# Performance work log

Hardware: AMD Instinct MI355X
Metric: run time of the kernel (lower is better)

## Reference

```python
import jax, jax.numpy as jnp
import numpy as np


def setup_inputs() -> dict:
    key = jax.random.key(0)
    k_x, k_q, k_k, k_v = jax.random.split(key, 4)
    B, S, D = 8, 1024, 768
    H, DH = 12, 64
    scale = 1.0 / np.sqrt(D)
    return {
        "x": jax.random.normal(k_x, (B, S, D), dtype=jnp.float32),
        "Wq": jax.random.normal(k_q, (H, D, DH), dtype=jnp.float32) * scale,
        "Wk": jax.random.normal(k_k, (H, D, DH), dtype=jnp.float32) * scale,
        "Wv": jax.random.normal(k_v, (H, D, DH), dtype=jnp.float32) * scale,
    }


def reference(x, Wq, Wk, Wv):
    # x: [B, S, D]; Wq/Wk/Wv: [H, D, DH] (per-head Linear weights, no bias)
    B, S, D = x.shape
    H, _, DH = Wq.shape
    q = jnp.einsum("bsd,hde->bhse", x, Wq)  # [B,H,S,DH]
    k = jnp.einsum("bsd,hde->bhse", x, Wk)
    v = jnp.einsum("bsd,hde->bhse", x, Wv)
    scores = jnp.einsum("bhse,bhte->bhst", q, k) / jnp.sqrt(jnp.float32(DH))
    causal = jnp.tril(jnp.ones((S, S), dtype=bool))  # keep lower triangle
    scores = jnp.where(causal, scores, -jnp.inf)
    attn = jax.nn.softmax(scores, axis=-1)  # dropout = 0.0 -> identity
    ctx = jnp.einsum("bhst,bhte->bhse", attn, v)  # [B,H,S,DH]
    # concat heads on last dim: [B,S,H*DH]
    return ctx.transpose(0, 2, 1, 3).reshape(B, S, H * DH)
```

## Files before the change

kernel.cpp:

```cpp
#include <hip/hip_runtime.h>


#define Bq 8
#define Sq 1024
#define Dq 768
#define Hq 12
#define DHq 64

typedef _Float16 f16;
typedef f16 f16x8 __attribute__((ext_vector_type(8)));
typedef float f32x4 __attribute__((ext_vector_type(4)));

#define MFMA16(a, b, c) __builtin_amdgcn_mfma_f32_16x16x32_f16(a, b, c, 0, 0, 0)

#define QSCL 0.1803368801111244f

#if __has_builtin(__builtin_amdgcn_exp2f)
#define EXP2(x) __builtin_amdgcn_exp2f(x)
#else
#define EXP2(x) exp2f(x)
#endif

__device__ __forceinline__ void gload16(const f16* g, f16* l) {
  __builtin_amdgcn_global_load_lds(
      (const __attribute__((address_space(1))) void*)g,
      (__attribute__((address_space(3))) void*)l, 16, 0, 0);
}

__global__ __launch_bounds__(256) void cvt_x_kernel(const float* __restrict__ x,
                                                    f16* __restrict__ xh) {
  int i = blockIdx.x * 256 + threadIdx.x;
  const float4* src = reinterpret_cast<const float4*>(x) + i * 2;
  float4 a = src[0], b = src[1];
  f16x8 o;
  o[0] = (f16)a.x; o[1] = (f16)a.y; o[2] = (f16)a.z; o[3] = (f16)a.w;
  o[4] = (f16)b.x; o[5] = (f16)b.y; o[6] = (f16)b.z; o[7] = (f16)b.w;
  *reinterpret_cast<f16x8*>(xh + i * 8) = o;
}

__global__ __launch_bounds__(256) void cvt_w_kernel(const float* __restrict__ Wq,
                                                    const float* __restrict__ Wk,
                                                    const float* __restrict__ Wv,
                                                    f16* __restrict__ WT) {
  __shared__ float tile[64][65];
  const int kt = blockIdx.x, h = blockIdx.y, w = blockIdx.z;
  const float* W = (w == 0) ? Wq : (w == 1) ? Wk : Wv;
  const int t = threadIdx.x;
  const int c0 = t & 63, r4 = t >> 6;
#pragma unroll
  for (int i = 0; i < 16; i++) {
    int kr = i * 4 + r4;
    tile[kr][c0] = W[((size_t)h * Dq + kt * 64 + kr) * DHq + c0];
  }
  __syncthreads();
#pragma unroll
  for (int i = 0; i < 16; i++) {
    int e2 = i * 4 + r4;
    WT[((size_t)(w * Hq + h) * DHq + e2) * Dq + kt * 64 + c0] = (f16)tile[c0][e2];
  }
}

__global__ __launch_bounds__(256) void proj_kernel(const f16* __restrict__ xh,
                                                   const f16* __restrict__ WT,
                                                   f16* __restrict__ Q,
                                                   f16* __restrict__ K,
                                                   f16* __restrict__ Vt) {
  __shared__ __align__(1024) f16 smem[30720];

  const int mt = blockIdx.x;
  const int h = blockIdx.y;
  const int row0 = mt * 128;
  const int t = threadIdx.x;
  const int wv = t >> 6;
  const int lane = t & 63;
  const int g = lane >> 4;
  const int ql = lane & 15;
  const int wvm = wv >> 1, wvn = wv & 1;

  const int lr = lane >> 2;
  const int scg = (lane & 3) ^ ((lane >> 3) & 3);

  const f16* xsrc = xh + (size_t)row0 * Dq;
  const f16* wsrc = WT + (size_t)h * DHq * Dq;

  const f16* gA0 = xsrc + (size_t)(wv * 32 + lr) * Dq + scg * 8;
  const f16* gA1 = gA0 + (size_t)16 * Dq;
  const int n0 = wv * 48 + lr, n1 = n0 + 16, n2 = n0 + 32;
  const f16* gB0 = wsrc + ((size_t)(n0 >> 6) * Hq * DHq + (n0 & 63)) * Dq + scg * 8;
  const f16* gB1 = wsrc + ((size_t)(n1 >> 6) * Hq * DHq + (n1 & 63)) * Dq + scg * 8;
  const f16* gB2 = wsrc + ((size_t)(n2 >> 6) * Hq * DHq + (n2 & 63)) * Dq + scg * 8;

  f32x4 acc[4][6] = {};

#define PROJ_STAGE(buf)                                              \
  do {                                                               \
    f16* sA_ = smem + (buf) * 4096 + wv * 1024;                      \
    f16* sB_ = smem + 12288 + (buf) * 6144 + wv * 1536;              \
    gload16(gA0, sA_); gload16(gA1, sA_ + 512);                      \
    gload16(gB0, sB_); gload16(gB1, sB_ + 512);                      \
    gload16(gB2, sB_ + 1024);                                        \
    gA0 += 32; gA1 += 32; gB0 += 32; gB1 += 32; gB2 += 32;           \
  } while (0)

  PROJ_STAGE(0);
  PROJ_STAGE(1);

  const int rq = (g ^ ((ql >> 1) & 3)) * 8;
  const f16* rA = smem + (wvm * 64 + ql) * 32 + rq;
  const f16* rB = smem + 12288 + (wvn * 96 + ql) * 32 + rq;

#pragma unroll
  for (int step = 0; step < 24; step++) {
    if (step < 23) asm volatile("s_waitcnt vmcnt(5) lgkmcnt(0)" ::: "memory");
    else           asm volatile("s_waitcnt vmcnt(0) lgkmcnt(0)" ::: "memory");
    __builtin_amdgcn_s_barrier();
    __builtin_amdgcn_sched_barrier(0);
    if (step < 22) PROJ_STAGE((step + 2) % 3);
    const int cur = step % 3;
    f16x8 af[4], bf[6];
#pragma unroll
    for (int mf = 0; mf < 4; mf++)
      af[mf] = *reinterpret_cast<const f16x8*>(rA + cur * 4096 + mf * 512);
#pragma unroll
    for (int nf = 0; nf < 6; nf++)
      bf[nf] = *reinterpret_cast<const f16x8*>(rB + cur * 6144 + nf * 512);
    __builtin_amdgcn_s_setprio(1);
#pragma unroll
    for (int mf = 0; mf < 4; mf++)
#pragma unroll
      for (int nf = 0; nf < 6; nf++)
        acc[mf][nf] = MFMA16(af[mf], bf[nf], acc[mf][nf]);
    __builtin_amdgcn_s_setprio(0);
  }
#undef PROJ_STAGE
  __syncthreads();

  const int b = row0 >> 10;
  const int s0 = row0 & 1023;
  const size_t base_sd = ((size_t)(b * Hq + h) * Sq) * DHq;

#pragma unroll
  for (int nf = 0; nf < 6; nf++) {
    const int c = wvn * 96 + nf * 16 + ql;
    const int w = c >> 6;
    if (w < 2) {
      f16* dst = (w == 0 ? Q : K);
      const float scl = (w == 0) ? QSCL : 1.0f;
      const int e = c & 63;
#pragma unroll
      for (int mf = 0; mf < 4; mf++) {
        const int sr = wvm * 64 + mf * 16 + g * 4;
#pragma unroll
        for (int r = 0; r < 4; r++)
          dst[base_sd + (size_t)(s0 + sr + r) * DHq + e] = (f16)(acc[mf][nf][r] * scl);
      }
    }
  }

  f16* vbuf = smem;
#pragma unroll
  for (int nf = 2; nf < 6; nf++) {
    if (wvn == 1) {
      const int e = (96 + nf * 16 + ql) & 63;
#pragma unroll
      for (int mf = 0; mf < 4; mf++) {
        const int sr = wvm * 64 + mf * 16 + g * 4;
        union { f16 hh[4]; uint2 u; } z;
#pragma unroll
        for (int r = 0; r < 4; r++) z.hh[r] = (f16)acc[mf][nf][r];
        *reinterpret_cast<uint2*>(&vbuf[e * 136 + sr]) = z.u;
      }
    }
  }
  __syncthreads();
#pragma unroll
  for (int i = 0; i < 4; i++) {
    int c = t + 256 * i;
    int e = c >> 4, p = (c & 15) * 8;
    *reinterpret_cast<uint4*>(Vt + base_sd + (size_t)e * Sq + s0 + p) =
        *reinterpret_cast<const uint4*>(vbuf + e * 136 + p);
  }
}

__global__ __launch_bounds__(256) void attn_kernel(const f16* __restrict__ Q,
                                                   const f16* __restrict__ K,
                                                   const f16* __restrict__ Vt,
                                                   float* __restrict__ out) {
  __shared__ __align__(16) f16 k_lds[2][64][72];
  __shared__ __align__(16) f16 vt_lds[2][64][72];

  const int L = blockIdx.x;
  const int i = L >> 3;
  const int bh = (L & 7) * Hq + (i % Hq);
  const int mt = 15 - (i / Hq);
  const int t = threadIdx.x;
  const int wv = t >> 6;
  const int lane = t & 63;
  const int g = lane >> 4;
  const int ql = lane & 15;

  const f16* Qb = Q + (size_t)bh * Sq * DHq;
  const f16* Kb = K + (size_t)bh * Sq * DHq;
  const f16* Vtb = Vt + (size_t)bh * DHq * Sq;
  const int b = bh / Hq, h = bh % Hq;

  const int r0 = t >> 3;
  const int p0 = (t & 7) * 8;

  const int q0 = mt * 64;
  const int qg = q0 + wv * 16 + ql;
  f16x8 qf0 = *reinterpret_cast<const f16x8*>(Qb + (size_t)qg * DHq + g * 8);
  f16x8 qf1 = *reinterpret_cast<const f16x8*>(Qb + (size_t)qg * DHq + 32 + g * 8);

  f32x4 o_acc[4] = {};
  float m_r = -__builtin_inff(), l_r = 0.f;

  uint4 kreg0, kreg1, vreg0, vreg1;
  kreg0 = *reinterpret_cast<const uint4*>(Kb + (size_t)r0 * DHq + p0);
  kreg1 = *reinterpret_cast<const uint4*>(Kb + (size_t)(32 + r0) * DHq + p0);
  vreg0 = *reinterpret_cast<const uint4*>(Vtb + (size_t)r0 * Sq + p0);
  vreg1 = *reinterpret_cast<const uint4*>(Vtb + (size_t)(32 + r0) * Sq + p0);
  *reinterpret_cast<uint4*>(&k_lds[0][r0][p0]) = kreg0;
  *reinterpret_cast<uint4*>(&k_lds[0][32 + r0][p0]) = kreg1;
  *reinterpret_cast<uint4*>(&vt_lds[0][r0][p0]) = vreg0;
  *reinterpret_cast<uint4*>(&vt_lds[0][32 + r0][p0]) = vreg1;
  if (mt >= 1) {
    kreg0 = *reinterpret_cast<const uint4*>(Kb + (size_t)(64 + r0) * DHq + p0);
    kreg1 = *reinterpret_cast<const uint4*>(Kb + (size_t)(96 + r0) * DHq + p0);
    vreg0 = *reinterpret_cast<const uint4*>(Vtb + (size_t)r0 * Sq + 64 + p0);
    vreg1 = *reinterpret_cast<const uint4*>(Vtb + (size_t)(32 + r0) * Sq + 64 + p0);
  }
  __syncthreads();

  int cur = 0;
  for (int kt = 0; kt <= mt; kt++) {
    f32x4 sf[4] = {};
    __builtin_amdgcn_s_setprio(1);
#pragma unroll
    for (int nt = 0; nt < 4; nt++) {
      f16x8 kf0 = *reinterpret_cast<const f16x8*>(&k_lds[cur][nt * 16 + ql][g * 8]);
      f16x8 kf1 = *reinterpret_cast<const f16x8*>(&k_lds[cur][nt * 16 + ql][32 + g * 8]);
      sf[nt] = MFMA16(kf0, qf0, sf[nt]);
      sf[nt] = MFMA16(kf1, qf1, sf[nt]);
    }
    __builtin_amdgcn_s_setprio(0);

    if (kt == mt) {
#pragma unroll
      for (int nt = 0; nt < 4; nt++)
#pragma unroll
        for (int r = 0; r < 4; r++)
          if (nt * 16 + g * 4 + r > wv * 16 + ql) sf[nt][r] = -__builtin_inff();
    }

    float t0 = fmaxf(fmaxf(sf[0][0], sf[0][1]), fmaxf(sf[0][2], sf[0][3]));
    float t1 = fmaxf(fmaxf(sf[1][0], sf[1][1]), fmaxf(sf[1][2], sf[1][3]));
    float t2 = fmaxf(fmaxf(sf[2][0], sf[2][1]), fmaxf(sf[2][2], sf[2][3]));
    float t3 = fmaxf(fmaxf(sf[3][0], sf[3][1]), fmaxf(sf[3][2], sf[3][3]));
    float rowmax = fmaxf(fmaxf(t0, t1), fmaxf(t2, t3));
    rowmax = fmaxf(rowmax, __shfl_xor(rowmax, 16, 64));
    rowmax = fmaxf(rowmax, __shfl_xor(rowmax, 32, 64));

    if (!__all(rowmax <= m_r + 8.f)) {
      float mnew = fmaxf(m_r, rowmax);
      float corr = EXP2(m_r - mnew);
      l_r *= corr;
#pragma unroll
      for (int nt = 0; nt < 4; nt++) {
        o_acc[nt][0] *= corr; o_acc[nt][1] *= corr;
        o_acc[nt][2] *= corr; o_acc[nt][3] *= corr;
      }
      m_r = mnew;
    }

    float p[4][4];
#pragma unroll
    for (int nt = 0; nt < 4; nt++)
#pragma unroll
      for (int r = 0; r < 4; r++) p[nt][r] = EXP2(sf[nt][r] - m_r);
    float s0 = (p[0][0] + p[0][1]) + (p[0][2] + p[0][3]);
    float s1 = (p[1][0] + p[1][1]) + (p[1][2] + p[1][3]);
    float s2 = (p[2][0] + p[2][1]) + (p[2][2] + p[2][3]);
    float s3 = (p[3][0] + p[3][1]) + (p[3][2] + p[3][3]);
    float rs = (s0 + s1) + (s2 + s3);
    rs += __shfl_xor(rs, 16, 64);
    rs += __shfl_xor(rs, 32, 64);
    l_r += rs;

    uint32_t pk[4][2];
#pragma unroll
    for (int nt = 0; nt < 4; nt++) {
      union { f16 hh[2]; uint32_t u; } z0, z1;
      z0.hh[0] = (f16)p[nt][0]; z0.hh[1] = (f16)p[nt][1];
      z1.hh[0] = (f16)p[nt][2]; z1.hh[1] = (f16)p[nt][3];
      pk[nt][0] = z0.u; pk[nt][1] = z1.u;
    }
    const int srcA = ((g & 1) * 2) * 16 + ql;
    const int srcB = srcA + 16;
    const bool selhi = (g >> 1) != 0;
    f16x8 pf[2];
#pragma unroll
    for (int ks = 0; ks < 2; ks++) {
      uint32_t aA0 = (uint32_t)__shfl((int)pk[2 * ks][0], srcA, 64);
      uint32_t aA1 = (uint32_t)__shfl((int)pk[2 * ks][1], srcA, 64);
      uint32_t aB0 = (uint32_t)__shfl((int)pk[2 * ks][0], srcB, 64);
      uint32_t aB1 = (uint32_t)__shfl((int)pk[2 * ks][1], srcB, 64);
      uint32_t bA0 = (uint32_t)__shfl((int)pk[2 * ks + 1][0], srcA, 64);
      uint32_t bA1 = (uint32_t)__shfl((int)pk[2 * ks + 1][1], srcA, 64);
      uint32_t bB0 = (uint32_t)__shfl((int)pk[2 * ks + 1][0], srcB, 64);
      uint32_t bB1 = (uint32_t)__shfl((int)pk[2 * ks + 1][1], srcB, 64);
      union { uint32_t w[4]; f16x8 v; } z;
      z.w[0] = selhi ? bA0 : aA0;
      z.w[1] = selhi ? bA1 : aA1;
      z.w[2] = selhi ? bB0 : aB0;
      z.w[3] = selhi ? bB1 : aB1;
      pf[ks] = z.v;
    }

    __builtin_amdgcn_s_setprio(1);
#pragma unroll
    for (int nt = 0; nt < 4; nt++) {
      f16x8 vf0 = *reinterpret_cast<const f16x8*>(&vt_lds[cur][nt * 16 + ql][g * 8]);
      f16x8 vf1 = *reinterpret_cast<const f16x8*>(&vt_lds[cur][nt * 16 + ql][32 + g * 8]);
      o_acc[nt] = MFMA16(vf0, pf[0], o_acc[nt]);
      o_acc[nt] = MFMA16(vf1, pf[1], o_acc[nt]);
    }
    __builtin_amdgcn_s_setprio(0);

    if (kt < mt) {
      *reinterpret_cast<uint4*>(&k_lds[cur ^ 1][r0][p0]) = kreg0;
      *reinterpret_cast<uint4*>(&k_lds[cur ^ 1][32 + r0][p0]) = kreg1;
      *reinterpret_cast<uint4*>(&vt_lds[cur ^ 1][r0][p0]) = vreg0;
      *reinterpret_cast<uint4*>(&vt_lds[cur ^ 1][32 + r0][p0]) = vreg1;
      if (kt + 2 <= mt) {
        const int kv0 = (kt + 2) * 64;
        kreg0 = *reinterpret_cast<const uint4*>(Kb + (size_t)(kv0 + r0) * DHq + p0);
        kreg1 = *reinterpret_cast<const uint4*>(Kb + (size_t)(kv0 + 32 + r0) * DHq + p0);
        vreg0 = *reinterpret_cast<const uint4*>(Vtb + (size_t)r0 * Sq + kv0 + p0);
        vreg1 = *reinterpret_cast<const uint4*>(Vtb + (size_t)(32 + r0) * Sq + kv0 + p0);
      }
    }
    __syncthreads();
    cur ^= 1;
  }

  float rl = 1.0f / l_r;
  float* op = out + ((size_t)(b * Sq + qg)) * (Hq * DHq) + h * DHq;
#pragma unroll
  for (int nt = 0; nt < 4; nt++) {
    float4 st = { o_acc[nt][0] * rl, o_acc[nt][1] * rl,
                  o_acc[nt][2] * rl, o_acc[nt][3] * rl };
    *reinterpret_cast<float4*>(op + nt * 16 + g * 4) = st;
  }
}

extern "C" void kernel_launch(void* const* d_in, const int* in_sizes, int n_in,
                              void* d_out, int out_size, void* d_ws, size_t ws_size,
                              hipStream_t stream) {
  const float* x = (const float*)d_in[0];
  const float* Wq = (const float*)d_in[1];
  const float* Wk = (const float*)d_in[2];
  const float* Wv = (const float*)d_in[3];
  float* out = (float*)d_out;

  const size_t off_xb = 0;
  const size_t off_wt = 12582912;
  const size_t off_q = 16121856;
  const size_t off_k = 28704768;
  const size_t off_v = 41287680;
  const size_t need = 53870592;
  if (ws_size < need) return;

  char* ws = (char*)d_ws;
  f16* xh = (f16*)(ws + off_xb);
  f16* WT = (f16*)(ws + off_wt);
  f16* Qd = (f16*)(ws + off_q);
  f16* Kd = (f16*)(ws + off_k);
  f16* Vtd = (f16*)(ws + off_v);

  cvt_x_kernel<<<3072, 256, 0, stream>>>(x, xh);
  cvt_w_kernel<<<dim3(12, 12, 3), 256, 0, stream>>>(Wq, Wk, Wv, WT);
  proj_kernel<<<dim3(64, 12), 256, 0, stream>>>(xh, WT, Qd, Kd, Vtd);
  attn_kernel<<<1536, 256, 0, stream>>>(Qd, Kd, Vtd, out);
}
```

Baseline: 86.35 us.

## Load K/V MFMA fragments directly from global memory, dropping LDS staging

```diff
diff --git a/kernel.cpp b/kernel.cpp
--- a/kernel.cpp
+++ b/kernel.cpp
@@ -186,9 +186,6 @@
                                                    const f16* __restrict__ K,
                                                    const f16* __restrict__ Vt,
                                                    float* __restrict__ out) {
-  __shared__ __align__(16) f16 k_lds[2][64][72];
-  __shared__ __align__(16) f16 vt_lds[2][64][72];
-
   const int L = blockIdx.x;
   const int i = L >> 3;
   const int bh = (L & 7) * Hq + (i % Hq);
@@ -204,44 +201,38 @@
   const f16* Vtb = Vt + (size_t)bh * DHq * Sq;
   const int b = bh / Hq, h = bh % Hq;
 
-  const int r0 = t >> 3;
-  const int p0 = (t & 7) * 8;
-
-  const int q0 = mt * 64;
-  const int qg = q0 + wv * 16 + ql;
+  const int qg = mt * 64 + wv * 16 + ql;
   f16x8 qf0 = *reinterpret_cast<const f16x8*>(Qb + (size_t)qg * DHq + g * 8);
   f16x8 qf1 = *reinterpret_cast<const f16x8*>(Qb + (size_t)qg * DHq + 32 + g * 8);
 
   f32x4 o_acc[4] = {};
   float m_r = -__builtin_inff(), l_r = 0.f;
 
-  uint4 kreg0, kreg1, vreg0, vreg1;
-  kreg0 = *reinterpret_cast<const uint4*>(Kb + (size_t)r0 * DHq + p0);
-  kreg1 = *reinterpret_cast<const uint4*>(Kb + (size_t)(32 + r0) * DHq + p0);
-  vreg0 = *reinterpret_cast<const uint4*>(Vtb + (size_t)r0 * Sq + p0);
-  vreg1 = *reinterpret_cast<const uint4*>(Vtb + (size_t)(32 + r0) * Sq + p0);
-  *reinterpret_cast<uint4*>(&k_lds[0][r0][p0]) = kreg0;
-  *reinterpret_cast<uint4*>(&k_lds[0][32 + r0][p0]) = kreg1;
-  *reinterpret_cast<uint4*>(&vt_lds[0][r0][p0]) = vreg0;
-  *reinterpret_cast<uint4*>(&vt_lds[0][32 + r0][p0]) = vreg1;
-  if (mt >= 1) {
-    kreg0 = *reinterpret_cast<const uint4*>(Kb + (size_t)(64 + r0) * DHq + p0);
-    kreg1 = *reinterpret_cast<const uint4*>(Kb + (size_t)(96 + r0) * DHq + p0);
-    vreg0 = *reinterpret_cast<const uint4*>(Vtb + (size_t)r0 * Sq + 64 + p0);
-    vreg1 = *reinterpret_cast<const uint4*>(Vtb + (size_t)(32 + r0) * Sq + 64 + p0);
-  }
-  __syncthreads();
-
-  int cur = 0;
+  const f16* kfb = Kb + (size_t)ql * DHq + g * 8;
+  const f16* vfb = Vtb + (size_t)ql * Sq + g * 8;
+
   for (int kt = 0; kt <= mt; kt++) {
+    const int kv0 = kt * 64;
+    f16x8 kf[4][2], vf[4][2];
+#pragma unroll
+    for (int nt = 0; nt < 4; nt++) {
+      const f16* kp = kfb + (size_t)(kv0 + nt * 16) * DHq;
+      kf[nt][0] = *reinterpret_cast<const f16x8*>(kp);
+      kf[nt][1] = *reinterpret_cast<const f16x8*>(kp + 32);
+    }
+#pragma unroll
+    for (int nt = 0; nt < 4; nt++) {
+      const f16* vp = vfb + (size_t)(nt * 16) * Sq + kv0;
+      vf[nt][0] = *reinterpret_cast<const f16x8*>(vp);
+      vf[nt][1] = *reinterpret_cast<const f16x8*>(vp + 32);
+    }
+
     f32x4 sf[4] = {};
     __builtin_amdgcn_s_setprio(1);
 #pragma unroll
     for (int nt = 0; nt < 4; nt++) {
-      f16x8 kf0 = *reinterpret_cast<const f16x8*>(&k_lds[cur][nt * 16 + ql][g * 8]);
-      f16x8 kf1 = *reinterpret_cast<const f16x8*>(&k_lds[cur][nt * 16 + ql][32 + g * 8]);
-      sf[nt] = MFMA16(kf0, qf0, sf[nt]);
-      sf[nt] = MFMA16(kf1, qf1, sf[nt]);
+      sf[nt] = MFMA16(kf[nt][0], qf0, sf[nt]);
+      sf[nt] = MFMA16(kf[nt][1], qf1, sf[nt]);
     }
     __builtin_amdgcn_s_setprio(0);
 
@@ -320,28 +311,10 @@
     __builtin_amdgcn_s_setprio(1);
 #pragma unroll
     for (int nt = 0; nt < 4; nt++) {
-      f16x8 vf0 = *reinterpret_cast<const f16x8*>(&vt_lds[cur][nt * 16 + ql][g * 8]);
-      f16x8 vf1 = *reinterpret_cast<const f16x8*>(&vt_lds[cur][nt * 16 + ql][32 + g * 8]);
-      o_acc[nt] = MFMA16(vf0, pf[0], o_acc[nt]);
-      o_acc[nt] = MFMA16(vf1, pf[1], o_acc[nt]);
+      o_acc[nt] = MFMA16(vf[nt][0], pf[0], o_acc[nt]);
+      o_acc[nt] = MFMA16(vf[nt][1], pf[1], o_acc[nt]);
     }
     __builtin_amdgcn_s_setprio(0);
-
-    if (kt < mt) {
-      *reinterpret_cast<uint4*>(&k_lds[cur ^ 1][r0][p0]) = kreg0;
-      *reinterpret_cast<uint4*>(&k_lds[cur ^ 1][32 + r0][p0]) = kreg1;
-      *reinterpret_cast<uint4*>(&vt_lds[cur ^ 1][r0][p0]) = vreg0;
-      *reinterpret_cast<uint4*>(&vt_lds[cur ^ 1][32 + r0][p0]) = vreg1;
-      if (kt + 2 <= mt) {
-        const int kv0 = (kt + 2) * 64;
-        kreg0 = *reinterpret_cast<const uint4*>(Kb + (size_t)(kv0 + r0) * DHq + p0);
-        kreg1 = *reinterpret_cast<const uint4*>(Kb + (size_t)(kv0 + 32 + r0) * DHq + p0);
-        vreg0 = *reinterpret_cast<const uint4*>(Vtb + (size_t)r0 * Sq + kv0 + p0);
-        vreg1 = *reinterpret_cast<const uint4*>(Vtb + (size_t)(32 + r0) * Sq + kv0 + p0);
-      }
-    }
-    __syncthreads();
-    cur ^= 1;
   }
 
   float rl = 1.0f / l_r;
```

After: 147.2 us. +70.5%, slower.

## Process two adjacent query tiles per attention block to reuse K/V tiles

Applied to the files above, without the earlier changes.

```diff
diff --git a/kernel.cpp b/kernel.cpp
--- a/kernel.cpp
+++ b/kernel.cpp
@@ -192,7 +192,8 @@
   const int L = blockIdx.x;
   const int i = L >> 3;
   const int bh = (L & 7) * Hq + (i % Hq);
-  const int mt = 15 - (i / Hq);
+  const int p = 7 - (i / Hq);
+  const int MT = 2 * p + 1;
   const int t = threadIdx.x;
   const int wv = t >> 6;
   const int lane = t & 63;
@@ -207,13 +208,17 @@
   const int r0 = t >> 3;
   const int p0 = (t & 7) * 8;
 
-  const int q0 = mt * 64;
-  const int qg = q0 + wv * 16 + ql;
-  f16x8 qf0 = *reinterpret_cast<const f16x8*>(Qb + (size_t)qg * DHq + g * 8);
-  f16x8 qf1 = *reinterpret_cast<const f16x8*>(Qb + (size_t)qg * DHq + 32 + g * 8);
-
-  f32x4 o_acc[4] = {};
-  float m_r = -__builtin_inff(), l_r = 0.f;
+  const int qg0 = 2 * p * 64 + wv * 16 + ql;
+  const int qg1 = qg0 + 64;
+  f16x8 qf[2][2];
+  qf[0][0] = *reinterpret_cast<const f16x8*>(Qb + (size_t)qg0 * DHq + g * 8);
+  qf[0][1] = *reinterpret_cast<const f16x8*>(Qb + (size_t)qg0 * DHq + 32 + g * 8);
+  qf[1][0] = *reinterpret_cast<const f16x8*>(Qb + (size_t)qg1 * DHq + g * 8);
+  qf[1][1] = *reinterpret_cast<const f16x8*>(Qb + (size_t)qg1 * DHq + 32 + g * 8);
+
+  f32x4 o_acc[2][4] = {};
+  float m_r[2] = { -__builtin_inff(), -__builtin_inff() };
+  float l_r[2] = { 0.f, 0.f };
 
   uint4 kreg0, kreg1, vreg0, vreg1;
   kreg0 = *reinterpret_cast<const uint4*>(Kb + (size_t)r0 * DHq + p0);
@@ -224,115 +229,122 @@
   *reinterpret_cast<uint4*>(&k_lds[0][32 + r0][p0]) = kreg1;
   *reinterpret_cast<uint4*>(&vt_lds[0][r0][p0]) = vreg0;
   *reinterpret_cast<uint4*>(&vt_lds[0][32 + r0][p0]) = vreg1;
-  if (mt >= 1) {
-    kreg0 = *reinterpret_cast<const uint4*>(Kb + (size_t)(64 + r0) * DHq + p0);
-    kreg1 = *reinterpret_cast<const uint4*>(Kb + (size_t)(96 + r0) * DHq + p0);
-    vreg0 = *reinterpret_cast<const uint4*>(Vtb + (size_t)r0 * Sq + 64 + p0);
-    vreg1 = *reinterpret_cast<const uint4*>(Vtb + (size_t)(32 + r0) * Sq + 64 + p0);
-  }
+  kreg0 = *reinterpret_cast<const uint4*>(Kb + (size_t)(64 + r0) * DHq + p0);
+  kreg1 = *reinterpret_cast<const uint4*>(Kb + (size_t)(96 + r0) * DHq + p0);
+  vreg0 = *reinterpret_cast<const uint4*>(Vtb + (size_t)r0 * Sq + 64 + p0);
+  vreg1 = *reinterpret_cast<const uint4*>(Vtb + (size_t)(32 + r0) * Sq + 64 + p0);
   __syncthreads();
 
   int cur = 0;
-  for (int kt = 0; kt <= mt; kt++) {
-    f32x4 sf[4] = {};
-    __builtin_amdgcn_s_setprio(1);
+  for (int kt = 0; kt <= MT; kt++) {
+    f16x8 kf[4][2], vf[4][2];
 #pragma unroll
     for (int nt = 0; nt < 4; nt++) {
-      f16x8 kf0 = *reinterpret_cast<const f16x8*>(&k_lds[cur][nt * 16 + ql][g * 8]);
-      f16x8 kf1 = *reinterpret_cast<const f16x8*>(&k_lds[cur][nt * 16 + ql][32 + g * 8]);
-      sf[nt] = MFMA16(kf0, qf0, sf[nt]);
-      sf[nt] = MFMA16(kf1, qf1, sf[nt]);
-    }
-    __builtin_amdgcn_s_setprio(0);
-
-    if (kt == mt) {
+      kf[nt][0] = *reinterpret_cast<const f16x8*>(&k_lds[cur][nt * 16 + ql][g * 8]);
+      kf[nt][1] = *reinterpret_cast<const f16x8*>(&k_lds[cur][nt * 16 + ql][32 + g * 8]);
+      vf[nt][0] = *reinterpret_cast<const f16x8*>(&vt_lds[cur][nt * 16 + ql][g * 8]);
+      vf[nt][1] = *reinterpret_cast<const f16x8*>(&vt_lds[cur][nt * 16 + ql][32 + g * 8]);
+    }
+
+#pragma unroll
+    for (int qs = 0; qs < 2; qs++) {
+      if (qs == 0 && kt > 2 * p) continue;
+      f32x4 sf[4] = {};
+      __builtin_amdgcn_s_setprio(1);
+#pragma unroll
+      for (int nt = 0; nt < 4; nt++) {
+        sf[nt] = MFMA16(kf[nt][0], qf[qs][0], sf[nt]);
+        sf[nt] = MFMA16(kf[nt][1], qf[qs][1], sf[nt]);
+      }
+      __builtin_amdgcn_s_setprio(0);
+
+      if (kt == 2 * p + qs) {
+#pragma unroll
+        for (int nt = 0; nt < 4; nt++)
+#pragma unroll
+          for (int r = 0; r < 4; r++)
+            if (nt * 16 + g * 4 + r > wv * 16 + ql) sf[nt][r] = -__builtin_inff();
+      }
+
+      float t0 = fmaxf(fmaxf(sf[0][0], sf[0][1]), fmaxf(sf[0][2], sf[0][3]));
+      float t1 = fmaxf(fmaxf(sf[1][0], sf[1][1]), fmaxf(sf[1][2], sf[1][3]));
+      float t2 = fmaxf(fmaxf(sf[2][0], sf[2][1]), fmaxf(sf[2][2], sf[2][3]));
+      float t3 = fmaxf(fmaxf(sf[3][0], sf[3][1]), fmaxf(sf[3][2], sf[3][3]));
+      float rowmax = fmaxf(fmaxf(t0, t1), fmaxf(t2, t3));
+      rowmax = fmaxf(rowmax, __shfl_xor(rowmax, 16, 64));
+      rowmax = fmaxf(rowmax, __shfl_xor(rowmax, 32, 64));
+
+      if (!__all(rowmax <= m_r[qs] + 8.f)) {
+        float mnew = fmaxf(m_r[qs], rowmax);
+        float corr = EXP2(m_r[qs] - mnew);
+        l_r[qs] *= corr;
+#pragma unroll
+        for (int nt = 0; nt < 4; nt++) {
+          o_acc[qs][nt][0] *= corr; o_acc[qs][nt][1] *= corr;
+          o_acc[qs][nt][2] *= corr; o_acc[qs][nt][3] *= corr;
+        }
+        m_r[qs] = mnew;
+      }
+
+      float pv[4][4];
 #pragma unroll
       for (int nt = 0; nt < 4; nt++)
 #pragma unroll
-        for (int r = 0; r < 4; r++)
-          if (nt * 16 + g * 4 + r > wv * 16 + ql) sf[nt][r] = -__builtin_inff();
-    }
-
-    float t0 = fmaxf(fmaxf(sf[0][0], sf[0][1]), fmaxf(sf[0][2], sf[0][3]));
-    float t1 = fmaxf(fmaxf(sf[1][0], sf[1][1]), fmaxf(sf[1][2], sf[1][3]));
-    float t2 = fmaxf(fmaxf(sf[2][0], sf[2][1]), fmaxf(sf[2][2], sf[2][3]));
-    float t3 = fmaxf(fmaxf(sf[3][0], sf[3][1]), fmaxf(sf[3][2], sf[3][3]));
-    float rowmax = fmaxf(fmaxf(t0, t1), fmaxf(t2, t3));
-    rowmax = fmaxf(rowmax, __shfl_xor(rowmax, 16, 64));
-    rowmax = fmaxf(rowmax, __shfl_xor(rowmax, 32, 64));
-
-    if (!__all(rowmax <= m_r + 8.f)) {
-      float mnew = fmaxf(m_r, rowmax);
-      float corr = EXP2(m_r - mnew);
-      l_r *= corr;
+        for (int r = 0; r < 4; r++) pv[nt][r] = EXP2(sf[nt][r] - m_r[qs]);
+      float s0 = (pv[0][0] + pv[0][1]) + (pv[0][2] + pv[0][3]);
+      float s1 = (pv[1][0] + pv[1][1]) + (pv[1][2] + pv[1][3]);
+      float s2 = (pv[2][0] + pv[2][1]) + (pv[2][2] + pv[2][3]);
+      float s3 = (pv[3][0] + pv[3][1]) + (pv[3][2] + pv[3][3]);
+      float rs = (s0 + s1) + (s2 + s3);
+      rs += __shfl_xor(rs, 16, 64);
+      rs += __shfl_xor(rs, 32, 64);
+      l_r[qs] += rs;
+
+      uint32_t pk[4][2];
 #pragma unroll
       for (int nt = 0; nt < 4; nt++) {
-        o_acc[nt][0] *= corr; o_acc[nt][1] *= corr;
-        o_acc[nt][2] *= corr; o_acc[nt][3] *= corr;
-      }
-      m_r = mnew;
-    }
-
-    float p[4][4];
-#pragma unroll
-    for (int nt = 0; nt < 4; nt++)
-#pragma unroll
-      for (int r = 0; r < 4; r++) p[nt][r] = EXP2(sf[nt][r] - m_r);
-    float s0 = (p[0][0] + p[0][1]) + (p[0][2] + p[0][3]);
-    float s1 = (p[1][0] + p[1][1]) + (p[1][2] + p[1][3]);
-    float s2 = (p[2][0] + p[2][1]) + (p[2][2] + p[2][3]);
-    float s3 = (p[3][0] + p[3][1]) + (p[3][2] + p[3][3]);
-    float rs = (s0 + s1) + (s2 + s3);
-    rs += __shfl_xor(rs, 16, 64);
-    rs += __shfl_xor(rs, 32, 64);
-    l_r += rs;
-
-    uint32_t pk[4][2];
-#pragma unroll
-    for (int nt = 0; nt < 4; nt++) {
-      union { f16 hh[2]; uint32_t u; } z0, z1;
-      z0.hh[0] = (f16)p[nt][0]; z0.hh[1] = (f16)p[nt][1];
-      z1.hh[0] = (f16)p[nt][2]; z1.hh[1] = (f16)p[nt][3];
-      pk[nt][0] = z0.u; pk[nt][1] = z1.u;
-    }
-    const int srcA = ((g & 1) * 2) * 16 + ql;
-    const int srcB = srcA + 16;
-    const bool selhi = (g >> 1) != 0;
-    f16x8 pf[2];
-#pragma unroll
-    for (int ks = 0; ks < 2; ks++) {
-      uint32_t aA0 = (uint32_t)__shfl((int)pk[2 * ks][0], srcA, 64);
-      uint32_t aA1 = (uint32_t)__shfl((int)pk[2 * ks][1], srcA, 64);
-      uint32_t aB0 = (uint32_t)__shfl((int)pk[2 * ks][0], srcB, 64);
-      uint32_t aB1 = (uint32_t)__shfl((int)pk[2 * ks][1], srcB, 64);
-      uint32_t bA0 = (uint32_t)__shfl((int)pk[2 * ks + 1][0], srcA, 64);
-      uint32_t bA1 = (uint32_t)__shfl((int)pk[2 * ks + 1][1], srcA, 64);
-      uint32_t bB0 = (uint32_t)__shfl((int)pk[2 * ks + 1][0], srcB, 64);
-      uint32_t bB1 = (uint32_t)__shfl((int)pk[2 * ks + 1][1], srcB, 64);
-      union { uint32_t w[4]; f16x8 v; } z;
-      z.w[0] = selhi ? bA0 : aA0;
-      z.w[1] = selhi ? bA1 : aA1;
-      z.w[2] = selhi ? bB0 : aB0;
-      z.w[3] = selhi ? bB1 : aB1;
-      pf[ks] = z.v;
-    }
-
-    __builtin_amdgcn_s_setprio(1);
-#pragma unroll
-    for (int nt = 0; nt < 4; nt++) {
-      f16x8 vf0 = *reinterpret_cast<const f16x8*>(&vt_lds[cur][nt * 16 + ql][g * 8]);
-      f16x8 vf1 = *reinterpret_cast<const f16x8*>(&vt_lds[cur][nt * 16 + ql][32 + g * 8]);
-      o_acc[nt] = MFMA16(vf0, pf[0], o_acc[nt]);
-      o_acc[nt] = MFMA16(vf1, pf[1], o_acc[nt]);
-    }
-    __builtin_amdgcn_s_setprio(0);
-
-    if (kt < mt) {
+        union { f16 hh[2]; uint32_t u; } z0, z1;
+        z0.hh[0] = (f16)pv[nt][0]; z0.hh[1] = (f16)pv[nt][1];
+        z1.hh[0] = (f16)pv[nt][2]; z1.hh[1] = (f16)pv[nt][3];
+        pk[nt][0] = z0.u; pk[nt][1] = z1.u;
+      }
+      const int srcA = ((g & 1) * 2) * 16 + ql;
+      const int srcB = srcA + 16;
+      const bool selhi = (g >> 1) != 0;
+      f16x8 pf[2];
+#pragma unroll
+      for (int ks = 0; ks < 2; ks++) {
+        uint32_t aA0 = (uint32_t)__shfl((int)pk[2 * ks][0], srcA, 64);
+        uint32_t aA1 = (uint32_t)__shfl((int)pk[2 * ks][1], srcA, 64);
+        uint32_t aB0 = (uint32_t)__shfl((int)pk[2 * ks][0], srcB, 64);
+        uint32_t aB1 = (uint32_t)__shfl((int)pk[2 * ks][1], srcB, 64);
+        uint32_t bA0 = (uint32_t)__shfl((int)pk[2 * ks + 1][0], srcA, 64);
+        uint32_t bA1 = (uint32_t)__shfl((int)pk[2 * ks + 1][1], srcA, 64);
+        uint32_t bB0 = (uint32_t)__shfl((int)pk[2 * ks + 1][0], srcB, 64);
+        uint32_t bB1 = (uint32_t)__shfl((int)pk[2 * ks + 1][1], srcB, 64);
+        union { uint32_t w[4]; f16x8 v; } z;
+        z.w[0] = selhi ? bA0 : aA0;
+        z.w[1] = selhi ? bA1 : aA1;
+        z.w[2] = selhi ? bB0 : aB0;
+        z.w[3] = selhi ? bB1 : aB1;
+        pf[ks] = z.v;
+      }
+
+      __builtin_amdgcn_s_setprio(1);
+#pragma unroll
+      for (int nt = 0; nt < 4; nt++) {
+        o_acc[qs][nt] = MFMA16(vf[nt][0], pf[0], o_acc[qs][nt]);
+        o_acc[qs][nt] = MFMA16(vf[nt][1], pf[1], o_acc[qs][nt]);
+      }
+      __builtin_amdgcn_s_setprio(0);
+    }
+
+    if (kt < MT) {
       *reinterpret_cast<uint4*>(&k_lds[cur ^ 1][r0][p0]) = kreg0;
       *reinterpret_cast<uint4*>(&k_lds[cur ^ 1][32 + r0][p0]) = kreg1;
       *reinterpret_cast<uint4*>(&vt_lds[cur ^ 1][r0][p0]) = vreg0;
       *reinterpret_cast<uint4*>(&vt_lds[cur ^ 1][32 + r0][p0]) = vreg1;
-      if (kt + 2 <= mt) {
+      if (kt + 2 <= MT) {
         const int kv0 = (kt + 2) * 64;
         kreg0 = *reinterpret_cast<const uint4*>(Kb + (size_t)(kv0 + r0) * DHq + p0);
         kreg1 = *reinterpret_cast<const uint4*>(Kb + (size_t)(kv0 + 32 + r0) * DHq + p0);
@@ -344,13 +356,17 @@
     cur ^= 1;
   }
 
-  float rl = 1.0f / l_r;
-  float* op = out + ((size_t)(b * Sq + qg)) * (Hq * DHq) + h * DHq;
-#pragma unroll
-  for (int nt = 0; nt < 4; nt++) {
-    float4 st = { o_acc[nt][0] * rl, o_acc[nt][1] * rl,
-                  o_acc[nt][2] * rl, o_acc[nt][3] * rl };
-    *reinterpret_cast<float4*>(op + nt * 16 + g * 4) = st;
+#pragma unroll
+  for (int qs = 0; qs < 2; qs++) {
+    const int qg = qs ? qg1 : qg0;
+    float rl = 1.0f / l_r[qs];
+    float* op = out + ((size_t)(b * Sq + qg)) * (Hq * DHq) + h * DHq;
+#pragma unroll
+    for (int nt = 0; nt < 4; nt++) {
+      float4 st = { o_acc[qs][nt][0] * rl, o_acc[qs][nt][1] * rl,
+                    o_acc[qs][nt][2] * rl, o_acc[qs][nt][3] * rl };
+      *reinterpret_cast<float4*>(op + nt * 16 + g * 4) = st;
+    }
   }
 }
 
@@ -381,5 +397,5 @@
   cvt_x_kernel<<<3072, 256, 0, stream>>>(x, xh);
   cvt_w_kernel<<<dim3(12, 12, 3), 256, 0, stream>>>(Wq, Wk, Wv, WT);
   proj_kernel<<<dim3(64, 12), 256, 0, stream>>>(xh, WT, Qd, Kd, Vtd);
-  attn_kernel<<<1536, 256, 0, stream>>>(Qd, Kd, Vtd, out);
-}
+  attn_kernel<<<768, 256, 0, stream>>>(Qd, Kd, Vtd, out);
+}
```

After: 89.33 us. 3.4% more time.
